# Kernel optimization log

Hardware: AMD Instinct MI355X
Metric: run time of the kernel (lower is better)

## Reference

```python
import jax, jax.numpy as jnp
import numpy as np

B, T, E, HD = 8, 2048, 1024, 64  # batch, seq (== n_ctx), n_embd, head_dim = n_embd // n_head


def setup_inputs() -> dict:
    key = jax.random.key(0)
    k1, k2, k3, k4 = jax.random.split(key, 4)
    x = jax.random.normal(k1, (B, T, E), dtype=jnp.float32)
    s = E ** -0.5  # Linear-like init scale
    Wq = jax.random.normal(k2, (E, HD), dtype=jnp.float32) * s
    Wk = jax.random.normal(k3, (E, HD), dtype=jnp.float32) * s
    Wv = jax.random.normal(k4, (E, HD), dtype=jnp.float32) * s
    return {"x": x, "Wq": Wq, "Wk": Wk, "Wv": Wv}


def reference(x, Wq, Wk, Wv):
    # q,k,v: [B, T, HD]
    q = jnp.einsum('bte,eh->bth', x, Wq)
    k = jnp.einsum('bte,eh->bth', x, Wk)
    v = jnp.einsum('bte,eh->bth', x, Wv)
    scale = k.shape[-1] ** -0.5
    # scores: [B, T, T]
    alpha = jnp.einsum('bqh,bkh->bqk', q, k) * scale
    causal = jnp.tril(jnp.ones((T, T), dtype=bool))
    alpha = jnp.where(causal, alpha, -jnp.inf)
    alpha = jax.nn.softmax(alpha, axis=-1)
    # dropout with p=0.0 is identity in eval
    h = jnp.einsum('bqk,bkh->bqh', alpha, v)  # [B, T, HD]
    return h
```

## Files before the change

kernel.cpp:

```cpp
#include <hip/hip_runtime.h>
#include <hip/hip_bf16.h>
#include <math.h>

#define BATCH 8
#define T 2048
#define E 1024
#define HD 64
#define BT (BATCH * T)

typedef __bf16 bf16_t;
typedef bf16_t bf16x4 __attribute__((ext_vector_type(4)));
typedef bf16_t bf16x8 __attribute__((ext_vector_type(8)));
typedef float f32x4 __attribute__((ext_vector_type(4)));

#define MFMA(a, b, c) __builtin_amdgcn_mfma_f32_16x16x32_bf16((a), (b), (c), 0, 0, 0)

#define QSCALE (0.125f * 1.44269504088896340736f)


__global__ __launch_bounds__(256) void prep_w(const float* __restrict__ Wq,
                                              const float* __restrict__ Wk,
                                              const float* __restrict__ Wv,
                                              bf16_t* __restrict__ WTt) {
    const int nt  = blockIdx.x >> 3;
    const int kc0 = (blockIdx.x & 7) * 128;
    const int tid = threadIdx.x;
    const int l16 = tid & 15;
    const int k8  = (kc0 >> 3) + (tid >> 4);
    const int n   = nt * 16 + l16;
    const int m   = n >> 6;
    const int col = n & 63;
    const float* W = (m == 0) ? Wq : (m == 1) ? Wk : Wv;
    const float scale = (m == 0) ? QSCALE : 1.0f;
    bf16x8 o;
#pragma unroll
    for (int j = 0; j < 8; j++) {
        o[j] = (bf16_t)(W[(size_t)(k8 * 8 + j) * HD + col] * scale);
    }
    *reinterpret_cast<bf16x8*>(WTt + (size_t)nt * 16384 + k8 * 128 + l16 * 8) = o;
}

__global__ __launch_bounds__(512, 2) void qkv_proj(
    const float* __restrict__ x,
    const bf16_t* __restrict__ WTt,
    bf16_t* __restrict__ qt,
    bf16_t* __restrict__ kt,
    bf16_t* __restrict__ vt)
{
    __shared__ __align__(16) bf16_t xb[64][1024];

    const int tid  = threadIdx.x;
    const int w    = tid >> 6;
    const int lane = tid & 63;
    const int l16  = lane & 15;
    const int quad = lane >> 4;
    const int wk   = w >> 2;
    const int wc   = w & 3;
    const int rowbase0 = blockIdx.x * 64;

    {
#pragma unroll
        for (int rd = 0; rd < 4; rd++) {
            f32x4 v[8];
#pragma unroll
            for (int j = 0; j < 8; j++) {
                const int gi = w * 32 + rd * 8 + j;
                const int r  = gi >> 2;
                const int q  = gi & 3;
                v[j] = *reinterpret_cast<const f32x4*>(
                    x + (size_t)(rowbase0 + r) * E + q * 256 + lane * 4);
            }
            __builtin_amdgcn_sched_barrier(0);
#pragma unroll
            for (int j = 0; j < 8; j++) {
                const int gi = w * 32 + rd * 8 + j;
                const int r  = gi >> 2;
                const int q  = gi & 3;
                bf16x4 w4;
#pragma unroll
                for (int u = 0; u < 4; u++) w4[u] = (bf16_t)v[j][u];
                char* base = reinterpret_cast<char*>(&xb[r][0]);
                const int off = (q * 512 + lane * 8) ^ ((r & 7) << 4);
                *reinterpret_cast<bf16x4*>(base + off) = w4;
            }
        }
    }
    __syncthreads();

    const bf16_t* Bb = WTt + (size_t)(wc * 3) * 16384 + lane * 8;
    f32x4 acc[4][3] = {};

    for (int kc8 = 0; kc8 < 8; kc8++) {
        const int kk = wk * 512 + kc8 * 64;
        bf16x8 bf[2][3];
#pragma unroll
        for (int ks = 0; ks < 2; ks++)
#pragma unroll
            for (int tc = 0; tc < 3; tc++)
                bf[ks][tc] = *reinterpret_cast<const bf16x8*>(
                    Bb + (size_t)tc * 16384 + (kk + ks * 32) * 16);

#pragma unroll
        for (int g = 0; g < 4; g++) {
            const int row = g * 16 + l16;
            const int swz = (row & 7) << 4;
            const char* rb = reinterpret_cast<const char*>(&xb[row][0]);
            const bf16x8 a0 = *reinterpret_cast<const bf16x8*>(
                rb + ((kk * 2 + quad * 16) ^ swz));
            const bf16x8 a1 = *reinterpret_cast<const bf16x8*>(
                rb + ((kk * 2 + 64 + quad * 16) ^ swz));
#pragma unroll
            for (int tc = 0; tc < 3; tc++) acc[g][tc] = MFMA(a0, bf[0][tc], acc[g][tc]);
#pragma unroll
            for (int tc = 0; tc < 3; tc++) acc[g][tc] = MFMA(a1, bf[1][tc], acc[g][tc]);
        }
    }

    __syncthreads();
    float* pbuf = reinterpret_cast<float*>(&xb[0][0]);
    if (wk == 1) {
#pragma unroll
        for (int g = 0; g < 4; g++)
#pragma unroll
            for (int tc = 0; tc < 3; tc++) {
                const int idx = (((wc * 4 + g) * 3) + tc) * 256 + lane * 4;
                *reinterpret_cast<f32x4*>(pbuf + idx) = acc[g][tc];
            }
    }
    __syncthreads();
    if (wk == 0) {
#pragma unroll
        for (int g = 0; g < 4; g++)
#pragma unroll
            for (int tc = 0; tc < 3; tc++) {
                const int idx = (((wc * 4 + g) * 3) + tc) * 256 + lane * 4;
                acc[g][tc] += *reinterpret_cast<const f32x4*>(pbuf + idx);
            }

#pragma unroll
        for (int g = 0; g < 4; g++) {
            const int rowbase = rowbase0 + g * 16;
#pragma unroll
            for (int tc = 0; tc < 3; tc++) {
                const int n0  = wc * 48 + tc * 16;
                const int m   = n0 >> 6;
                const int tcg = (n0 & 63) >> 4;
                if (m < 2) {
                    bf16_t* dst = (m == 0) ? qt : kt;
                    const size_t o0 = (size_t)(rowbase >> 4) * 1024 +
                                      (size_t)(tcg * 2 + (l16 >> 3)) * 128 + (l16 & 7);
#pragma unroll
                    for (int r = 0; r < 4; r++) {
                        dst[o0 + (quad * 4 + r) * 8] = (bf16_t)acc[g][tc][r];
                    }
                } else {
                    const int b_    = rowbase >> 11;
                    const int tbase = rowbase & (T - 1);
                    const size_t o0 = (size_t)b_ * 131072 +
                                      (size_t)((tbase >> 3) + (quad >> 1)) * 128 +
                                      l16 * 8 + (quad & 1) * 4 + (size_t)tcg * 32768;
                    bf16x4 pv;
#pragma unroll
                    for (int r = 0; r < 4; r++) pv[r] = (bf16_t)acc[g][tc][r];
                    *reinterpret_cast<bf16x4*>(vt + o0) = pv;
                }
            }
        }
    }
}

__global__ __launch_bounds__(512, 2) void attn(
    const bf16_t* __restrict__ qtl,
    const bf16_t* __restrict__ ktl,
    const bf16_t* __restrict__ vtl,
    float* __restrict__ out)
{
    __shared__ __align__(16) bf16_t plds[8][16][40];
    __shared__ float opart[8][16][66];
    __shared__ float lpart[8][16];

    const int wave = threadIdx.x >> 6;
    const int lane = threadIdx.x & 63;
    const int l16  = lane & 15;
    const int quad = lane >> 4;
    const int group = wave >> 2;
    const int kw    = wave & 3;

    const int b  = blockIdx.x >> 6;
    const int pr = blockIdx.x & 63;
    const int qt = group ? (127 - pr) : pr;
    const int rowbase = qt * 16;

    const bf16_t* Qb = qtl + (size_t)((b * T + rowbase) >> 4) * 1024 + lane * 8;
    const bf16_t* Kb = ktl + (size_t)b * T * 64 + lane * 8;
    const bf16_t* Vb = vtl + (size_t)b * 131072 + lane * 8;

    const bf16x8 qf0 = *reinterpret_cast<const bf16x8*>(Qb);
    const bf16x8 qf1 = *reinterpret_cast<const bf16x8*>(Qb + 512);

    f32x4 o[4] = {};
    f32x4 lrun = {};

    const int nch = (rowbase + 47) >> 5;

    int k0 = kw * 32;
    bf16x8 kfa0 = *reinterpret_cast<const bf16x8*>(Kb + k0 * 64);
    bf16x8 kfb0 = *reinterpret_cast<const bf16x8*>(Kb + k0 * 64 + 512);
    bf16x8 kfa1 = *reinterpret_cast<const bf16x8*>(Kb + k0 * 64 + 1024);
    bf16x8 kfb1 = *reinterpret_cast<const bf16x8*>(Kb + k0 * 64 + 1536);
    bf16x8 vf0 = *reinterpret_cast<const bf16x8*>(Vb + k0 * 16);
    bf16x8 vf1 = *reinterpret_cast<const bf16x8*>(Vb + k0 * 16 + 32768);
    bf16x8 vf2 = *reinterpret_cast<const bf16x8*>(Vb + k0 * 16 + 65536);
    bf16x8 vf3 = *reinterpret_cast<const bf16x8*>(Vb + k0 * 16 + 98304);

    for (int c = kw; c < nch; c += 4) {
        k0 = c * 32;
        const int cn = (c + 4 < nch) ? (c + 4) : c;
        const int kn = cn * 32;
        bf16x8 nkfa0 = *reinterpret_cast<const bf16x8*>(Kb + kn * 64);
        bf16x8 nkfb0 = *reinterpret_cast<const bf16x8*>(Kb + kn * 64 + 512);
        bf16x8 nkfa1 = *reinterpret_cast<const bf16x8*>(Kb + kn * 64 + 1024);
        bf16x8 nkfb1 = *reinterpret_cast<const bf16x8*>(Kb + kn * 64 + 1536);
        bf16x8 nvf0 = *reinterpret_cast<const bf16x8*>(Vb + kn * 16);
        bf16x8 nvf1 = *reinterpret_cast<const bf16x8*>(Vb + kn * 16 + 32768);
        bf16x8 nvf2 = *reinterpret_cast<const bf16x8*>(Vb + kn * 16 + 65536);
        bf16x8 nvf3 = *reinterpret_cast<const bf16x8*>(Vb + kn * 16 + 98304);

        f32x4 s_lo = {};
        f32x4 s_hi = {};
        s_lo = MFMA(qf0, kfa0, s_lo);
        s_lo = MFMA(qf1, kfb0, s_lo);
        s_hi = MFMA(qf0, kfa1, s_hi);
        s_hi = MFMA(qf1, kfb1, s_hi);

        if (k0 + 31 > rowbase) {
            const int row = rowbase + quad * 4;
#pragma unroll
            for (int r = 0; r < 4; r++) {
                if (k0 + l16 > row + r)      s_lo[r] = -INFINITY;
                if (k0 + 16 + l16 > row + r) s_hi[r] = -INFINITY;
            }
        }

#pragma unroll
        for (int r = 0; r < 4; r++) {
            const float p0 = exp2f(s_lo[r]);
            const float p1 = exp2f(s_hi[r]);
            lrun[r] += p0 + p1;
            plds[wave][quad * 4 + r][l16]      = (bf16_t)p0;
            plds[wave][quad * 4 + r][16 + l16] = (bf16_t)p1;
        }
        const bf16x8 pf = *reinterpret_cast<const bf16x8*>(&plds[wave][l16][quad * 8]);

        o[0] = MFMA(pf, vf0, o[0]);
        o[1] = MFMA(pf, vf1, o[1]);
        o[2] = MFMA(pf, vf2, o[2]);
        o[3] = MFMA(pf, vf3, o[3]);

        kfa0 = nkfa0; kfb0 = nkfb0; kfa1 = nkfa1; kfb1 = nkfb1;
        vf0 = nvf0; vf1 = nvf1; vf2 = nvf2; vf3 = nvf3;
    }

#pragma unroll
    for (int r = 0; r < 4; r++) {
        float l = lrun[r];
        l += __shfl_xor(l, 1);
        l += __shfl_xor(l, 2);
        l += __shfl_xor(l, 4);
        l += __shfl_xor(l, 8);
        if (l16 == 0) lpart[wave][quad * 4 + r] = l;
#pragma unroll
        for (int nb = 0; nb < 4; nb++) {
            opart[wave][quad * 4 + r][nb * 16 + l16] = o[nb][r];
        }
    }
    __syncthreads();

    const int g    = threadIdx.x >> 8;
    const int gtid = threadIdx.x & 255;
    const int qtg  = g ? (127 - pr) : pr;
    const size_t outbase = (size_t)b * T + qtg * 16;
#pragma unroll
    for (int pass = 0; pass < 4; pass++) {
        const int row = pass * 4 + (gtid >> 6);
        const int col = gtid & 63;
        float osum = 0.f, lsum = 0.f;
#pragma unroll
        for (int w = 0; w < 4; w++) {
            osum += opart[g * 4 + w][row][col];
            lsum += lpart[g * 4 + w][row];
        }
        out[(outbase + row) * HD + col] = osum / lsum;
    }
}

extern "C" void kernel_launch(void* const* d_in, const int* in_sizes, int n_in,
                              void* d_out, int out_size, void* d_ws, size_t ws_size,
                              hipStream_t stream) {
    const float* x  = (const float*)d_in[0];
    const float* Wq = (const float*)d_in[1];
    const float* Wk = (const float*)d_in[2];
    const float* Wv = (const float*)d_in[3];
    float* out = (float*)d_out;

    bf16_t* ws  = (bf16_t*)d_ws;
    bf16_t* WTt = ws;
    bf16_t* qtl = WTt + (size_t)192 * E;
    bf16_t* ktl = qtl + (size_t)BT * HD;
    bf16_t* vtl = ktl + (size_t)BT * HD;

    prep_w<<<96, 256, 0, stream>>>(Wq, Wk, Wv, WTt);
    qkv_proj<<<256, 512, 0, stream>>>(x, WTt, qtl, ktl, vtl);
    attn<<<512, 512, 0, stream>>>(qtl, ktl, vtl, out);
}
```

Baseline: 119.4 us.

## Overlap second-half x staging with first-half MFMA in qkv_proj

The x tile load into shared memory is split into two K-halves. All warps first stage half 0. Warp group 0 then runs its MFMAs on it while warp group 1 loads and converts half 1, and group 1 computes after a barrier. The aim is to hide global-load latency behind compute. In exchange, load work is now uneven across warps, and group 1's compute is serialized after group 0's load window.

```diff
diff --git a/kernel.cpp b/kernel.cpp
--- a/kernel.cpp
+++ b/kernel.cpp
@@ -47,7 +47,7 @@
     bf16_t* __restrict__ kt,
     bf16_t* __restrict__ vt)
 {
-    __shared__ __align__(16) bf16_t xb[64][1024];
+    __shared__ __align__(16) bf16_t xb[2][64][512];
 
     const int tid  = threadIdx.x;
     const int w    = tid >> 6;
@@ -58,66 +58,106 @@
     const int wc   = w & 3;
     const int rowbase0 = blockIdx.x * 64;
 
+    const bf16_t* Bb = WTt + (size_t)(wc * 3) * 16384 + lane * 8;
+    f32x4 acc[4][3] = {};
+
     {
+#pragma unroll
+        for (int rd = 0; rd < 2; rd++) {
+            f32x4 v[8];
+#pragma unroll
+            for (int j = 0; j < 8; j++) {
+                const int gi = w * 16 + rd * 8 + j;
+                const int r  = gi >> 1;
+                const int hh = gi & 1;
+                v[j] = *reinterpret_cast<const f32x4*>(
+                    x + (size_t)(rowbase0 + r) * E + hh * 256 + lane * 4);
+            }
+            __builtin_amdgcn_sched_barrier(0);
+#pragma unroll
+            for (int j = 0; j < 8; j++) {
+                const int gi = w * 16 + rd * 8 + j;
+                const int r  = gi >> 1;
+                const int hh = gi & 1;
+                bf16x4 w4;
+#pragma unroll
+                for (int u = 0; u < 4; u++) w4[u] = (bf16_t)v[j][u];
+                char* base = reinterpret_cast<char*>(&xb[0][r][0]);
+                const int off = (hh * 512 + lane * 8) ^ ((r & 7) << 4);
+                *reinterpret_cast<bf16x4*>(base + off) = w4;
+            }
+        }
+    }
+    __syncthreads();
+
+#define QKV_COMPUTE(h)                                                        \
+    for (int kc8 = 0; kc8 < 8; kc8++) {                                       \
+        const int kkg = (h) * 512 + kc8 * 64;                                 \
+        const int kkl = kc8 * 64;                                             \
+        bf16x8 bfrag[2][3];                                                   \
+        _Pragma("unroll")                                                     \
+        for (int ks = 0; ks < 2; ks++)                                        \
+            _Pragma("unroll")                                                 \
+            for (int tc = 0; tc < 3; tc++)                                    \
+                bfrag[ks][tc] = *reinterpret_cast<const bf16x8*>(             \
+                    Bb + (size_t)tc * 16384 + (kkg + ks * 32) * 16);          \
+        _Pragma("unroll")                                                     \
+        for (int g = 0; g < 4; g++) {                                         \
+            const int row = g * 16 + l16;                                     \
+            const int swz = (row & 7) << 4;                                   \
+            const char* rb = reinterpret_cast<const char*>(&xb[h][row][0]);   \
+            const bf16x8 a0 = *reinterpret_cast<const bf16x8*>(               \
+                rb + ((kkl * 2 + quad * 16) ^ swz));                          \
+            const bf16x8 a1 = *reinterpret_cast<const bf16x8*>(               \
+                rb + ((kkl * 2 + 64 + quad * 16) ^ swz));                     \
+            _Pragma("unroll")                                                 \
+            for (int tc = 0; tc < 3; tc++)                                    \
+                acc[g][tc] = MFMA(a0, bfrag[0][tc], acc[g][tc]);              \
+            _Pragma("unroll")                                                 \
+            for (int tc = 0; tc < 3; tc++)                                    \
+                acc[g][tc] = MFMA(a1, bfrag[1][tc], acc[g][tc]);              \
+        }                                                                     \
+    }
+
+    if (wk == 0) {
+        QKV_COMPUTE(0)
+    } else {
+        const int wl = w - 4;
 #pragma unroll
         for (int rd = 0; rd < 4; rd++) {
             f32x4 v[8];
 #pragma unroll
             for (int j = 0; j < 8; j++) {
-                const int gi = w * 32 + rd * 8 + j;
-                const int r  = gi >> 2;
-                const int q  = gi & 3;
+                const int gi = wl * 32 + rd * 8 + j;
+                const int r  = gi >> 1;
+                const int hh = gi & 1;
                 v[j] = *reinterpret_cast<const f32x4*>(
-                    x + (size_t)(rowbase0 + r) * E + q * 256 + lane * 4);
+                    x + (size_t)(rowbase0 + r) * E + 512 + hh * 256 + lane * 4);
             }
             __builtin_amdgcn_sched_barrier(0);
 #pragma unroll
             for (int j = 0; j < 8; j++) {
-                const int gi = w * 32 + rd * 8 + j;
-                const int r  = gi >> 2;
-                const int q  = gi & 3;
+                const int gi = wl * 32 + rd * 8 + j;
+                const int r  = gi >> 1;
+                const int hh = gi & 1;
                 bf16x4 w4;
 #pragma unroll
                 for (int u = 0; u < 4; u++) w4[u] = (bf16_t)v[j][u];
-                char* base = reinterpret_cast<char*>(&xb[r][0]);
-                const int off = (q * 512 + lane * 8) ^ ((r & 7) << 4);
+                char* base = reinterpret_cast<char*>(&xb[1][r][0]);
+                const int off = (hh * 512 + lane * 8) ^ ((r & 7) << 4);
                 *reinterpret_cast<bf16x4*>(base + off) = w4;
             }
         }
     }
     __syncthreads();
 
-    const bf16_t* Bb = WTt + (size_t)(wc * 3) * 16384 + lane * 8;
-    f32x4 acc[4][3] = {};
-
-    for (int kc8 = 0; kc8 < 8; kc8++) {
-        const int kk = wk * 512 + kc8 * 64;
-        bf16x8 bf[2][3];
-#pragma unroll
-        for (int ks = 0; ks < 2; ks++)
-#pragma unroll
-            for (int tc = 0; tc < 3; tc++)
-                bf[ks][tc] = *reinterpret_cast<const bf16x8*>(
-                    Bb + (size_t)tc * 16384 + (kk + ks * 32) * 16);
-
-#pragma unroll
-        for (int g = 0; g < 4; g++) {
-            const int row = g * 16 + l16;
-            const int swz = (row & 7) << 4;
-            const char* rb = reinterpret_cast<const char*>(&xb[row][0]);
-            const bf16x8 a0 = *reinterpret_cast<const bf16x8*>(
-                rb + ((kk * 2 + quad * 16) ^ swz));
-            const bf16x8 a1 = *reinterpret_cast<const bf16x8*>(
-                rb + ((kk * 2 + 64 + quad * 16) ^ swz));
-#pragma unroll
-            for (int tc = 0; tc < 3; tc++) acc[g][tc] = MFMA(a0, bf[0][tc], acc[g][tc]);
-#pragma unroll
-            for (int tc = 0; tc < 3; tc++) acc[g][tc] = MFMA(a1, bf[1][tc], acc[g][tc]);
-        }
-    }
-
-    __syncthreads();
-    float* pbuf = reinterpret_cast<float*>(&xb[0][0]);
+    if (wk == 1) {
+        QKV_COMPUTE(1)
+    }
+    __syncthreads();
+#undef QKV_COMPUTE
+
+    float* pbuf = reinterpret_cast<float*>(&xb[0][0][0]);
     if (wk == 1) {
 #pragma unroll
         for (int g = 0; g < 4; g++)
```

Result: slower. 122.3 us (+2.4%).

## Process two 32-row query tile pairs per block, sharing K/V loads across 8 waves

Applied to the files above, without the earlier changes.

Each block now handles two 32-row query tiles (a balanced causal pair) instead of two 16-row tiles, so each loaded K/V chunk feeds two 16-row MFMA groups. All 8 waves split the combined 65 key chunks of both tiles in a flat task list, which balances causal work within the block, and the grid is halved to 256 blocks. The aim is to cut K/V global traffic per query row and raise MFMA work per load. In exchange, V is no longer prefetched a step ahead, there are more accumulator registers, and the result merge now runs four serialized reductions, each followed by a block barrier.

```diff
diff --git a/kernel.cpp b/kernel.cpp
--- a/kernel.cpp
+++ b/kernel.cpp
@@ -175,123 +175,159 @@
     const bf16_t* __restrict__ vtl,
     float* __restrict__ out)
 {
-    __shared__ __align__(16) bf16_t plds[8][16][40];
+    __shared__ __align__(16) bf16_t plds[8][2][16][40];
     __shared__ float opart[8][16][66];
     __shared__ float lpart[8][16];
 
-    const int wave = threadIdx.x >> 6;
-    const int lane = threadIdx.x & 63;
+    const int tid  = threadIdx.x;
+    const int wave = tid >> 6;
+    const int lane = tid & 63;
     const int l16  = lane & 15;
     const int quad = lane >> 4;
-    const int group = wave >> 2;
-    const int kw    = wave & 3;
-
-    const int b  = blockIdx.x >> 6;
-    const int pr = blockIdx.x & 63;
-    const int qt = group ? (127 - pr) : pr;
-    const int rowbase = qt * 16;
-
-    const bf16_t* Qb = qtl + (size_t)((b * T + rowbase) >> 4) * 1024 + lane * 8;
+
+    const int b  = blockIdx.x >> 5;
+    const int pp = blockIdx.x & 31;
+    const int rbA = pp * 32;
+    const int rbB = (63 - pp) * 32;
+    const int nchA = pp + 1;
+
     const bf16_t* Kb = ktl + (size_t)b * T * 64 + lane * 8;
     const bf16_t* Vb = vtl + (size_t)b * 131072 + lane * 8;
-
-    const bf16x8 qf0 = *reinterpret_cast<const bf16x8*>(Qb);
-    const bf16x8 qf1 = *reinterpret_cast<const bf16x8*>(Qb + 512);
-
-    f32x4 o[4] = {};
-    f32x4 lrun = {};
-
-    const int nch = (rowbase + 47) >> 5;
-
-    int k0 = kw * 32;
-    bf16x8 kfa0 = *reinterpret_cast<const bf16x8*>(Kb + k0 * 64);
-    bf16x8 kfb0 = *reinterpret_cast<const bf16x8*>(Kb + k0 * 64 + 512);
-    bf16x8 kfa1 = *reinterpret_cast<const bf16x8*>(Kb + k0 * 64 + 1024);
-    bf16x8 kfb1 = *reinterpret_cast<const bf16x8*>(Kb + k0 * 64 + 1536);
-    bf16x8 vf0 = *reinterpret_cast<const bf16x8*>(Vb + k0 * 16);
-    bf16x8 vf1 = *reinterpret_cast<const bf16x8*>(Vb + k0 * 16 + 32768);
-    bf16x8 vf2 = *reinterpret_cast<const bf16x8*>(Vb + k0 * 16 + 65536);
-    bf16x8 vf3 = *reinterpret_cast<const bf16x8*>(Vb + k0 * 16 + 98304);
-
-    for (int c = kw; c < nch; c += 4) {
+    const bf16_t* QbA = qtl + (size_t)((b * T + rbA) >> 4) * 1024 + lane * 8;
+    const bf16_t* QbB = qtl + (size_t)((b * T + rbB) >> 4) * 1024 + lane * 8;
+
+    const bf16x8 qA0l = *reinterpret_cast<const bf16x8*>(QbA);
+    const bf16x8 qA0h = *reinterpret_cast<const bf16x8*>(QbA + 512);
+    const bf16x8 qA1l = *reinterpret_cast<const bf16x8*>(QbA + 1024);
+    const bf16x8 qA1h = *reinterpret_cast<const bf16x8*>(QbA + 1536);
+    const bf16x8 qB0l = *reinterpret_cast<const bf16x8*>(QbB);
+    const bf16x8 qB0h = *reinterpret_cast<const bf16x8*>(QbB + 512);
+    const bf16x8 qB1l = *reinterpret_cast<const bf16x8*>(QbB + 1024);
+    const bf16x8 qB1h = *reinterpret_cast<const bf16x8*>(QbB + 1536);
+
+    f32x4 oA0[4] = {}, oA1[4] = {}, oB0[4] = {}, oB1[4] = {};
+    f32x4 lrA0 = {}, lrA1 = {}, lrB0 = {}, lrB1 = {};
+
+    int k0;
+    bf16x8 kfa0, kfb0, kfa1, kfb1;
+    {
+        const int tf = wave;
+        const int cf = (tf < nchA) ? tf : tf - nchA;
+        kfa0 = *reinterpret_cast<const bf16x8*>(Kb + cf * 32 * 64);
+        kfb0 = *reinterpret_cast<const bf16x8*>(Kb + cf * 32 * 64 + 512);
+        kfa1 = *reinterpret_cast<const bf16x8*>(Kb + cf * 32 * 64 + 1024);
+        kfb1 = *reinterpret_cast<const bf16x8*>(Kb + cf * 32 * 64 + 1536);
+    }
+
+#define ATTN_STEP(QL0, QH0, QL1, QH1, RB_, O0, O1, LR0, LR1)                  \
+    {                                                                         \
+        f32x4 s0l = {}, s0h = {}, s1l = {}, s1h = {};                         \
+        s0l = MFMA(QL0, kfa0, s0l);  s0l = MFMA(QH0, kfb0, s0l);              \
+        s0h = MFMA(QL0, kfa1, s0h);  s0h = MFMA(QH0, kfb1, s0h);              \
+        s1l = MFMA(QL1, kfa0, s1l);  s1l = MFMA(QH1, kfb0, s1l);              \
+        s1h = MFMA(QL1, kfa1, s1h);  s1h = MFMA(QH1, kfb1, s1h);              \
+        if (k0 + 31 > (RB_)) {                                                \
+            const int row = (RB_) + quad * 4;                                 \
+            _Pragma("unroll")                                                 \
+            for (int r = 0; r < 4; r++) {                                     \
+                if (k0 + l16 > row + r)      s0l[r] = -INFINITY;              \
+                if (k0 + 16 + l16 > row + r) s0h[r] = -INFINITY;              \
+            }                                                                 \
+        }                                                                     \
+        if (k0 + 31 > (RB_) + 16) {                                           \
+            const int row = (RB_) + 16 + quad * 4;                            \
+            _Pragma("unroll")                                                 \
+            for (int r = 0; r < 4; r++) {                                     \
+                if (k0 + l16 > row + r)      s1l[r] = -INFINITY;              \
+                if (k0 + 16 + l16 > row + r) s1h[r] = -INFINITY;              \
+            }                                                                 \
+        }                                                                     \
+        _Pragma("unroll")                                                     \
+        for (int r = 0; r < 4; r++) {                                         \
+            const float p00 = exp2f(s0l[r]);                                  \
+            const float p01 = exp2f(s0h[r]);                                  \
+            (LR0)[r] += p00 + p01;                                            \
+            plds[wave][0][quad * 4 + r][l16]      = (bf16_t)p00;              \
+            plds[wave][0][quad * 4 + r][16 + l16] = (bf16_t)p01;              \
+            const float p10 = exp2f(s1l[r]);                                  \
+            const float p11 = exp2f(s1h[r]);                                  \
+            (LR1)[r] += p10 + p11;                                            \
+            plds[wave][1][quad * 4 + r][l16]      = (bf16_t)p10;              \
+            plds[wave][1][quad * 4 + r][16 + l16] = (bf16_t)p11;              \
+        }                                                                     \
+        const bf16x8 pf0 = *reinterpret_cast<const bf16x8*>(                  \
+            &plds[wave][0][l16][quad * 8]);                                   \
+        const bf16x8 pf1 = *reinterpret_cast<const bf16x8*>(                  \
+            &plds[wave][1][l16][quad * 8]);                                   \
+        (O0)[0] = MFMA(pf0, vf0, (O0)[0]);  (O1)[0] = MFMA(pf1, vf0, (O1)[0]);\
+        (O0)[1] = MFMA(pf0, vf1, (O0)[1]);  (O1)[1] = MFMA(pf1, vf1, (O1)[1]);\
+        (O0)[2] = MFMA(pf0, vf2, (O0)[2]);  (O1)[2] = MFMA(pf1, vf2, (O1)[2]);\
+        (O0)[3] = MFMA(pf0, vf3, (O0)[3]);  (O1)[3] = MFMA(pf1, vf3, (O1)[3]);\
+    }
+
+    for (int task = wave; task < 65; task += 8) {
+        const bool isA = task < nchA;
+        const int  c   = isA ? task : task - nchA;
         k0 = c * 32;
-        const int cn = (c + 4 < nch) ? (c + 4) : c;
+
+        const bf16x8 vf0 = *reinterpret_cast<const bf16x8*>(Vb + k0 * 16);
+        const bf16x8 vf1 = *reinterpret_cast<const bf16x8*>(Vb + k0 * 16 + 32768);
+        const bf16x8 vf2 = *reinterpret_cast<const bf16x8*>(Vb + k0 * 16 + 65536);
+        const bf16x8 vf3 = *reinterpret_cast<const bf16x8*>(Vb + k0 * 16 + 98304);
+        const int tn = (task + 8 < 65) ? task + 8 : task;
+        const int cn = (tn < nchA) ? tn : tn - nchA;
         const int kn = cn * 32;
-        bf16x8 nkfa0 = *reinterpret_cast<const bf16x8*>(Kb + kn * 64);
-        bf16x8 nkfb0 = *reinterpret_cast<const bf16x8*>(Kb + kn * 64 + 512);
-        bf16x8 nkfa1 = *reinterpret_cast<const bf16x8*>(Kb + kn * 64 + 1024);
-        bf16x8 nkfb1 = *reinterpret_cast<const bf16x8*>(Kb + kn * 64 + 1536);
-        bf16x8 nvf0 = *reinterpret_cast<const bf16x8*>(Vb + kn * 16);
-        bf16x8 nvf1 = *reinterpret_cast<const bf16x8*>(Vb + kn * 16 + 32768);
-        bf16x8 nvf2 = *reinterpret_cast<const bf16x8*>(Vb + kn * 16 + 65536);
-        bf16x8 nvf3 = *reinterpret_cast<const bf16x8*>(Vb + kn * 16 + 98304);
-
-        f32x4 s_lo = {};
-        f32x4 s_hi = {};
-        s_lo = MFMA(qf0, kfa0, s_lo);
-        s_lo = MFMA(qf1, kfb0, s_lo);
-        s_hi = MFMA(qf0, kfa1, s_hi);
-        s_hi = MFMA(qf1, kfb1, s_hi);
-
-        if (k0 + 31 > rowbase) {
-            const int row = rowbase + quad * 4;
-#pragma unroll
-            for (int r = 0; r < 4; r++) {
-                if (k0 + l16 > row + r)      s_lo[r] = -INFINITY;
-                if (k0 + 16 + l16 > row + r) s_hi[r] = -INFINITY;
-            }
+        const bf16x8 nkfa0 = *reinterpret_cast<const bf16x8*>(Kb + kn * 64);
+        const bf16x8 nkfb0 = *reinterpret_cast<const bf16x8*>(Kb + kn * 64 + 512);
+        const bf16x8 nkfa1 = *reinterpret_cast<const bf16x8*>(Kb + kn * 64 + 1024);
+        const bf16x8 nkfb1 = *reinterpret_cast<const bf16x8*>(Kb + kn * 64 + 1536);
+
+        if (isA) {
+            ATTN_STEP(qA0l, qA0h, qA1l, qA1h, rbA, oA0, oA1, lrA0, lrA1)
+        } else {
+            ATTN_STEP(qB0l, qB0h, qB1l, qB1h, rbB, oB0, oB1, lrB0, lrB1)
         }
 
-#pragma unroll
-        for (int r = 0; r < 4; r++) {
-            const float p0 = exp2f(s_lo[r]);
-            const float p1 = exp2f(s_hi[r]);
-            lrun[r] += p0 + p1;
-            plds[wave][quad * 4 + r][l16]      = (bf16_t)p0;
-            plds[wave][quad * 4 + r][16 + l16] = (bf16_t)p1;
-        }
-        const bf16x8 pf = *reinterpret_cast<const bf16x8*>(&plds[wave][l16][quad * 8]);
-
-        o[0] = MFMA(pf, vf0, o[0]);
-        o[1] = MFMA(pf, vf1, o[1]);
-        o[2] = MFMA(pf, vf2, o[2]);
-        o[3] = MFMA(pf, vf3, o[3]);
-
         kfa0 = nkfa0; kfb0 = nkfb0; kfa1 = nkfa1; kfb1 = nkfb1;
-        vf0 = nvf0; vf1 = nvf1; vf2 = nvf2; vf3 = nvf3;
-    }
-
-#pragma unroll
-    for (int r = 0; r < 4; r++) {
-        float l = lrun[r];
-        l += __shfl_xor(l, 1);
-        l += __shfl_xor(l, 2);
-        l += __shfl_xor(l, 4);
-        l += __shfl_xor(l, 8);
-        if (l16 == 0) lpart[wave][quad * 4 + r] = l;
-#pragma unroll
-        for (int nb = 0; nb < 4; nb++) {
-            opart[wave][quad * 4 + r][nb * 16 + l16] = o[nb][r];
-        }
-    }
-    __syncthreads();
-
-    const int g    = threadIdx.x >> 8;
-    const int gtid = threadIdx.x & 255;
-    const int qtg  = g ? (127 - pr) : pr;
-    const size_t outbase = (size_t)b * T + qtg * 16;
-#pragma unroll
-    for (int pass = 0; pass < 4; pass++) {
-        const int row = pass * 4 + (gtid >> 6);
-        const int col = gtid & 63;
-        float osum = 0.f, lsum = 0.f;
-#pragma unroll
-        for (int w = 0; w < 4; w++) {
-            osum += opart[g * 4 + w][row][col];
-            lsum += lpart[g * 4 + w][row];
-        }
-        out[(outbase + row) * HD + col] = osum / lsum;
-    }
+    }
+#undef ATTN_STEP
+
+#define DEPOSIT_MERGE(OX, LRX, ROWBASE)                                       \
+    {                                                                         \
+        _Pragma("unroll")                                                     \
+        for (int r = 0; r < 4; r++) {                                         \
+            float l = (LRX)[r];                                               \
+            l += __shfl_xor(l, 1); l += __shfl_xor(l, 2);                     \
+            l += __shfl_xor(l, 4); l += __shfl_xor(l, 8);                     \
+            if (l16 == 0) lpart[wave][quad * 4 + r] = l;                      \
+            _Pragma("unroll")                                                 \
+            for (int nb = 0; nb < 4; nb++)                                    \
+                opart[wave][quad * 4 + r][nb * 16 + l16] = (OX)[nb][r];       \
+        }                                                                     \
+        __syncthreads();                                                      \
+        {                                                                     \
+            const int col = tid & 63;                                         \
+            const int rh  = tid >> 6;                                         \
+            _Pragma("unroll")                                                 \
+            for (int pass = 0; pass < 2; pass++) {                            \
+                const int row = pass * 8 + rh;                                \
+                float osum = 0.f, lsum = 0.f;                                 \
+                _Pragma("unroll")                                             \
+                for (int w2 = 0; w2 < 8; w2++) {                              \
+                    osum += opart[w2][row][col];                              \
+                    lsum += lpart[w2][row];                                   \
+                }                                                             \
+                out[((size_t)b * T + (ROWBASE) + row) * HD + col] = osum / lsum; \
+            }                                                                 \
+        }                                                                     \
+        __syncthreads();                                                      \
+    }
+
+    DEPOSIT_MERGE(oA0, lrA0, rbA)
+    DEPOSIT_MERGE(oA1, lrA1, rbA + 16)
+    DEPOSIT_MERGE(oB0, lrB0, rbB)
+    DEPOSIT_MERGE(oB1, lrB1, rbB + 16)
+#undef DEPOSIT_MERGE
 }
 
 extern "C" void kernel_launch(void* const* d_in, const int* in_sizes, int n_in,
@@ -311,5 +347,5 @@
 
     prep_w<<<96, 256, 0, stream>>>(Wq, Wk, Wv, WTt);
     qkv_proj<<<256, 512, 0, stream>>>(x, WTt, qtl, ktl, vtl);
-    attn<<<512, 512, 0, stream>>>(qtl, ktl, vtl, out);
+    attn<<<256, 512, 0, stream>>>(qtl, ktl, vtl, out);
 }
```

New measurement: 119.2 us (median of 2 runs). About the same (-0.2%).
